# Kernel optimization log

Hardware: AMD Instinct MI355X
Metric: run time of the kernel (lower is better)

## Reference

```python
import jax, jax.numpy as jnp
import numpy as np


def _make_grid(h, w):
    """Replicates gen_grid_coordinates_optimized(h, w, stride=1) vectorized in numpy.
    Returns (h*3, w*3, 2) float32 grid in grid_sample convention (x=col, y=row, in [-1,1])."""
    pi = np.pi
    dphi = pi / h
    dtheta = 2 * pi / w
    tp, tt, icp = np.tan(dphi), np.tan(dtheta), 1.0 / np.cos(dphi)
    xys = np.array([[(-tt, icp * tp), (0, tp), (tt, icp * tp)],
                    [(-tt, 0), (1, 1), (tt, 0)],
                    [(-tt, -icp * tp), (0, -tp), (tt, -icp * tp)]], dtype=np.float64)
    xk, yk = xys[..., 0], xys[..., 1]          # (3,3) kernel offsets on tangent plane
    rho = np.sqrt(xk ** 2 + yk ** 2)
    v = np.arctan(rho)
    cv, sv = np.cos(v), np.sin(v)
    rr = np.arange(h, dtype=np.float64)
    cc = np.arange(w, dtype=np.float64)
    phi = -((rr + 0.5) / h * pi - pi / 2)      # (h,)
    theta = (cc + 0.5) / w * 2 * pi - pi       # (w,)
    cph = np.cos(phi)[:, None, None]
    sph = np.sin(phi)[:, None, None]
    # (h,3,3) ; clip guards fp roundoff at poles (mathematically |arg|<=1)
    new_phi = np.arcsin(np.clip(cv * sph + yk * sv * cph / rho, -1.0, 1.0))
    dtheta_off = np.arctan(xk * sv / (rho * cph * cv - yk * sph * sv))  # (h,3,3)
    new_theta = theta[None, :, None, None] + dtheta_off[:, None]        # (h,w,3,3)
    new_r = np.broadcast_to(((-new_phi + pi / 2) * h / pi - 0.5)[:, None], (h, w, 3, 3)).copy()
    new_c = (new_theta + pi) * w / (2 * pi) - 0.5
    new_c = (new_c + w) % w
    # kernel center samples the pixel itself
    new_r[:, :, 1, 1] = rr[:, None]
    new_c[:, :, 1, 1] = cc[None, :]
    gy = new_r * 2 / h - 1
    gx = new_c * 2 / w - 1
    grid = np.stack([gx, gy], axis=-1)                      # (h,w,ki,kj,2)
    grid = grid.transpose(0, 2, 1, 3, 4).reshape(h * 3, w * 3, 2)
    return grid.astype(np.float32)


def _grid_sample_bilinear(x, grid):
    """F.grid_sample(mode='bilinear', align_corners=True, padding_mode='zeros').
    x: (N,C,H,W), grid: (Hg,Wg,2) shared across batch. Returns (N,C,Hg,Wg)."""
    N, C, H, W = x.shape
    ix = (grid[..., 0] + 1) * 0.5 * (W - 1)
    iy = (grid[..., 1] + 1) * 0.5 * (H - 1)
    x0 = jnp.floor(ix)
    y0 = jnp.floor(iy)
    x1, y1 = x0 + 1, y0 + 1
    xflat = x.reshape(N, C, H * W)

    def corner(yc, xc, wgt):
        valid = (xc >= 0) & (xc <= W - 1) & (yc >= 0) & (yc <= H - 1)
        xi = jnp.clip(xc, 0, W - 1).astype(jnp.int32)
        yi = jnp.clip(yc, 0, H - 1).astype(jnp.int32)
        idx = (yi * W + xi).reshape(-1)
        v = xflat[:, :, idx].reshape(N, C, *xc.shape)
        return v * (wgt * valid)[None, None]

    out = (corner(y0, x0, (x1 - ix) * (y1 - iy))
           + corner(y0, x1, (ix - x0) * (y1 - iy))
           + corner(y1, x0, (x1 - ix) * (iy - y0))
           + corner(y1, x1, (ix - x0) * (iy - y0)))
    return out


def setup_inputs() -> dict:
    key = jax.random.key(0)
    k1, k2 = jax.random.split(key)
    B, Cin, Cout, H, W = 4, 16, 32, 256, 512
    x = jax.random.normal(k1, (B, Cin, H, W), dtype=jnp.float32)
    fan_out = Cout * 9  # kaiming_normal fan_out, relu gain
    weight = jax.random.normal(k2, (Cout, Cin, 3, 3), dtype=jnp.float32) * np.sqrt(2.0 / fan_out)
    bias = jnp.zeros((Cout,), dtype=jnp.float32)
    grid = jnp.asarray(_make_grid(H, W))  # (H*3, W*3, 2) constant spherical warp
    return {"x": x, "weight": weight, "bias": bias, "grid": grid}


def reference(x, weight, bias, grid):
    s = _grid_sample_bilinear(x, grid)  # (N,C,3H,3W)
    out = jax.lax.conv_general_dilated(
        s, weight, window_strides=(3, 3), padding='VALID',
        dimension_numbers=('NCHW', 'OIHW', 'NCHW'))
    return out + bias[None, :, None, None]
```

## Files before the change

### kernel.cpp

```cpp
#include <hip/hip_runtime.h>

#define HH 256
#define WW 512
#define NCIN 16
#define NCOUT 32
#define NB 4
#define WKP 168

typedef _Float16 half8 __attribute__((ext_vector_type(8)));
typedef float f32x16 __attribute__((ext_vector_type(16)));

#define XT_OFF   0u
#define XTAB_OFF 16777216u
#define WTAB_OFF (16777216u + 9437184u)
#define YTAB_OFF (16777216u + 9437184u + 16384u)
#define WS_NEED  (YTAB_OFF + 36864u)

__global__ __launch_bounds__(256) void precompute_all(const float* __restrict__ x,
                                                      const float* __restrict__ w,
                                                      const float* __restrict__ grid,
                                                      _Float16* __restrict__ xh,
                                                      float2* __restrict__ xtab,
                                                      _Float16* __restrict__ wtab,
                                                      float4* __restrict__ ytab) {
    const float2* g2 = reinterpret_cast<const float2*>(grid);
    if (blockIdx.x < 2048) {
        const int lb = (blockIdx.x & 7) * 256 + (blockIdx.x >> 3);
        const int t = lb * 256 + threadIdx.x;
        const int c = t & (WW - 1);
        const int r = (t >> 9) & (HH - 1);
        const int b = t >> 17;
        const float* xp = x + ((size_t)(b * NCIN) * HH + r) * WW + c;
        half8 h0, h1;
#pragma unroll
        for (int ci = 0; ci < 8; ++ci)  h0[ci] = (_Float16)xp[(size_t)ci * (HH * WW)];
#pragma unroll
        for (int ci = 0; ci < 8; ++ci)  h1[ci] = (_Float16)xp[(size_t)(8 + ci) * (HH * WW)];
        half8* op = reinterpret_cast<half8*>(xh) + (size_t)t * 2;
        op[0] = h0;
        op[1] = h1;
        return;
    }
    if (blockIdx.x < 2048 + 4608) {
        const int t = (blockIdx.x - 2048) * 256 + threadIdx.x;
        const int c = t & (WW - 1);
        const int u = t >> 9;
        const int r = u / 9, tap = u - r * 9;
        const int kr = tap / 3, kc = tap - kr * 3;
        const float gx = g2[(size_t)(r * 3 + kr) * (WW * 3) + (c * 3 + kc)].x;
        const float ix = ((gx + 1.0f) * 0.5f) * (float)(WW - 1);
        const float x0f = floorf(ix);
        xtab[t] = make_float2(ix - x0f, __int_as_float((int)x0f));
        return;
    }
    const int t = (blockIdx.x - 6656) * 256 + threadIdx.x;
    if (t < NCOUT * WKP) {
        const int co = t / WKP, kk = t - co * WKP;
        float v = 0.0f;
        if (kk < 144) v = w[co * 144 + (kk & 15) * 9 + (kk >> 4)];
        wtab[t] = (_Float16)v;
    } else if (t < NCOUT * WKP + HH * 9) {
        const int u = t - NCOUT * WKP;
        const int r = u / 9, tap = u - r * 9;
        const int kr = tap / 3, kc = tap - kr * 3;
        const float gy = g2[(size_t)(r * 3 + kr) * (WW * 3) + kc].y;
        const float iy = ((gy + 1.0f) * 0.5f) * (float)(HH - 1);
        const float y0f = floorf(iy);
        const float fy = iy - y0f;
        const int y0 = (int)y0f, y1 = y0 + 1;
        float wy0 = 1.0f - fy, wy1 = fy;
        if (y0 < 0 || y0 > HH - 1) wy0 = 0.0f;
        if (y1 < 0 || y1 > HH - 1) wy1 = 0.0f;
        const int cy0 = min(max(y0, 0), HH - 1), cy1 = min(max(y1, 0), HH - 1);
        ytab[u] = make_float4(wy0, wy1, __int_as_float(cy0), __int_as_float(cy1));
    }
}

__global__ __launch_bounds__(256, 4) void sphere_mfma_kernel(const _Float16* __restrict__ xh,
                                                             const float2* __restrict__ xtab,
                                                             const _Float16* __restrict__ wtab,
                                                             const float4* __restrict__ ytab,
                                                             const float* __restrict__ bias,
                                                             float* __restrict__ out) {
    const int tid = threadIdx.x, lane = tid & 63, wv = tid >> 6;
    const int c32 = lane & 31, h = lane >> 5;
    const int px = wv * 32 + c32;

    const int lb = ((blockIdx.x & 7) << 9) + (blockIdx.x >> 3);
    const int pixbase = lb << 7;
    const int b    = pixbase >> 17;
    const int rimg = (pixbase >> 9) & (HH - 1);
    const int c0   = pixbase & (WW - 1);

    float wy0s[9], wy1s[9];
    int Rb0[9], Rb1[9];
#pragma unroll
    for (int t = 0; t < 9; ++t) {
        const float4 y = ytab[rimg * 9 + t];
        wy0s[t] = y.x;
        wy1s[t] = y.y;
        Rb0[t] = (b * HH + __float_as_int(y.z)) << 10;
        Rb1[t] = (b * HH + __float_as_int(y.w)) << 10;
    }

    const float2* xrow = xtab + (size_t)rimg * 9 * WW + (c0 + px);
    float2 f2s[9];
#pragma unroll
    for (int t = 0; t < 9; ++t) f2s[t] = xrow[t * WW];

    half8 wA[9];
#pragma unroll
    for (int t = 0; t < 9; ++t)
        wA[t] = *reinterpret_cast<const half8*>(wtab + c32 * WKP + t * 16 + h * 8);

    const half8* x8 = reinterpret_cast<const half8*>(xh);
    f32x16 acc = {};
#pragma unroll
    for (int t = 0; t < 9; ++t) {
        const int x0 = __float_as_int(f2s[t].y);
        const int pb0 = Rb0[t] + (x0 << 1) + h;
        const int pb1 = Rb1[t] + (x0 << 1) + h;
        const half8 A00 = x8[pb0];
        const half8 A01 = x8[pb0 + 2];
        const half8 A10 = x8[pb1];
        const half8 A11 = x8[pb1 + 2];

        const float fx = f2s[t].x;
        const float wx0 = 1.0f - fx;
        const float w00 = wx0 * wy0s[t], w01 = fx * wy0s[t];
        const float w10 = wx0 * wy1s[t], w11 = fx * wy1s[t];
        const _Float16 W00 = (_Float16)w00, W01 = (_Float16)w01;
        const _Float16 W10 = (_Float16)w10, W11 = (_Float16)w11;
        const half8 B00 = {W00, W00, W00, W00, W00, W00, W00, W00};
        const half8 B01 = {W01, W01, W01, W01, W01, W01, W01, W01};
        const half8 B10 = {W10, W10, W10, W10, W10, W10, W10, W10};
        const half8 B11 = {W11, W11, W11, W11, W11, W11, W11, W11};
        half8 pk = A00 * B00;
        pk += A01 * B01;
        pk += A10 * B10;
        pk += A11 * B11;

        acc = __builtin_amdgcn_mfma_f32_32x32x16_f16(wA[t], pk, acc, 0, 0, 0);
    }

    const int pix = c0 + wv * 32 + c32;
    float* ob = out + (((size_t)(b * NCOUT) * HH + rimg) * WW) + pix;
#pragma unroll
    for (int reg = 0; reg < 16; ++reg) {
        const int co = (reg & 3) + 8 * (reg >> 2) + 4 * h;
        ob[(size_t)co * (HH * WW)] = acc[reg] + bias[co];
    }
}

__global__ __launch_bounds__(256) void sphere_conv_fallback(const float* __restrict__ x,
                                                            const float* __restrict__ weight,
                                                            const float* __restrict__ bias,
                                                            const float* __restrict__ grid,
                                                            float* __restrict__ out) {
    __shared__ float wlds[NCIN * 9 * NCOUT];
    const int tid = threadIdx.x;
    for (int e = tid; e < NCIN * 9 * NCOUT; e += 256) {
        const int co  = e & (NCOUT - 1);
        const int cik = e >> 5;
        wlds[e] = weight[co * (NCIN * 9) + cik];
    }
    __syncthreads();

    const int pindex = blockIdx.x * 256 + tid;
    const int c = pindex & (WW - 1);
    const int r = (pindex >> 9) & (HH - 1);
    const int b = pindex >> 17;

    float acc[NCOUT];
#pragma unroll
    for (int o = 0; o < NCOUT; ++o) acc[o] = 0.0f;

    const float2* g2 = reinterpret_cast<const float2*>(grid);

#pragma unroll 1
    for (int k = 0; k < 9; ++k) {
        const int kr = k / 3, kc = k - kr * 3;
        const float2 g = g2[(r * 3 + kr) * (WW * 3) + (c * 3 + kc)];
        const float ix = ((g.x + 1.0f) * 0.5f) * (float)(WW - 1);
        const float iy = ((g.y + 1.0f) * 0.5f) * (float)(HH - 1);
        const float x0f = floorf(ix), y0f = floorf(iy);
        const float fx = ix - x0f, fy = iy - y0f;
        const int x0 = (int)x0f, y0 = (int)y0f;
        const int x1 = x0 + 1, y1 = y0 + 1;
        float wx0 = 1.0f - fx, wx1 = fx, wy0 = 1.0f - fy, wy1 = fy;
        if (x0 < 0 || x0 > WW - 1) wx0 = 0.0f;
        if (x1 < 0 || x1 > WW - 1) wx1 = 0.0f;
        if (y0 < 0 || y0 > HH - 1) wy0 = 0.0f;
        if (y1 < 0 || y1 > HH - 1) wy1 = 0.0f;
        const int cx0 = min(max(x0, 0), WW - 1), cx1 = min(max(x1, 0), WW - 1);
        const int cy0 = min(max(y0, 0), HH - 1), cy1 = min(max(y1, 0), HH - 1);
        const float w00 = wx0 * wy0, w01 = wx1 * wy0, w10 = wx0 * wy1, w11 = wx1 * wy1;

#pragma unroll 1
        for (int ci = 0; ci < NCIN; ++ci) {
            const float* xb = x + (size_t)((b * NCIN + ci) * HH) * WW;
            const float a00 = xb[cy0 * WW + cx0];
            const float a01 = xb[cy0 * WW + cx1];
            const float a10 = xb[cy1 * WW + cx0];
            const float a11 = xb[cy1 * WW + cx1];
            const float s = w00 * a00 + w01 * a01 + w10 * a10 + w11 * a11;
            const float4* wl = reinterpret_cast<const float4*>(&wlds[(ci * 9 + k) * NCOUT]);
#pragma unroll
            for (int o = 0; o < 8; ++o) {
                const float4 wv = wl[o];
                acc[o * 4 + 0] += wv.x * s;
                acc[o * 4 + 1] += wv.y * s;
                acc[o * 4 + 2] += wv.z * s;
                acc[o * 4 + 3] += wv.w * s;
            }
        }
    }

    const int obase = ((b * NCOUT) * HH + r) * WW + c;
#pragma unroll
    for (int o = 0; o < NCOUT; ++o) {
        out[obase + o * (HH * WW)] = acc[o] + bias[o];
    }
}

extern "C" void kernel_launch(void* const* d_in, const int* in_sizes, int n_in,
                              void* d_out, int out_size, void* d_ws, size_t ws_size,
                              hipStream_t stream) {
    const float* x    = (const float*)d_in[0];
    const float* w    = (const float*)d_in[1];
    const float* bias = (const float*)d_in[2];
    const float* grid = (const float*)d_in[3];
    float* out = (float*)d_out;

    if (ws_size >= WS_NEED) {
        char* ws = (char*)d_ws;
        _Float16* xh   = (_Float16*)(ws + XT_OFF);
        float2*   xtab = (float2*)(ws + XTAB_OFF);
        _Float16* wtab = (_Float16*)(ws + WTAB_OFF);
        float4*   ytab = (float4*)(ws + YTAB_OFF);

        precompute_all<<<6686, 256, 0, stream>>>(x, w, grid, xh, xtab, wtab, ytab);
        sphere_mfma_kernel<<<4096, 256, 0, stream>>>(xh, xtab, wtab, ytab, bias, out);
    } else {
        sphere_conv_fallback<<<2048, 256, 0, stream>>>(x, w, bias, grid, out);
    }
}
```

Before: 55.40 us.

## Double-buffer gather loads, coalesce grid reads, pre-swizzle MFMA weight fragments

The main kernel's tap loop is now software-pipelined with two register buffers, so the four corner gathers for tap t+2 are issued while tap t is blended and fed to the MFMA. The precompute pass now reads the grid coalesced and scatters into the xtab layout, instead of the strided gather it did before. Weights are also pre-packed into the per-lane MFMA fragment order so each lane does one contiguous half8 load. The pipelining raises register pressure under the 4-blocks-per-CU launch bound, and the xtab writes become scattered.

```diff
diff --git a/kernel.cpp b/kernel.cpp
--- a/kernel.cpp
+++ b/kernel.cpp
@@ -5,14 +5,13 @@
 #define NCIN 16
 #define NCOUT 32
 #define NB 4
-#define WKP 168
 
 typedef _Float16 half8 __attribute__((ext_vector_type(8)));
 typedef float f32x16 __attribute__((ext_vector_type(16)));
 
 #define XT_OFF   0u
 #define XTAB_OFF 16777216u
-#define WTAB_OFF (16777216u + 9437184u)
+#define WFRAG_OFF (16777216u + 9437184u)
 #define YTAB_OFF (16777216u + 9437184u + 16384u)
 #define WS_NEED  (YTAB_OFF + 36864u)
 
@@ -21,7 +20,7 @@
                                                       const float* __restrict__ grid,
                                                       _Float16* __restrict__ xh,
                                                       float2* __restrict__ xtab,
-                                                      _Float16* __restrict__ wtab,
+                                                      _Float16* __restrict__ wfrag,
                                                       float4* __restrict__ ytab) {
     const float2* g2 = reinterpret_cast<const float2*>(grid);
     if (blockIdx.x < 2048) {
@@ -41,29 +40,29 @@
         op[1] = h1;
         return;
     }
-    if (blockIdx.x < 2048 + 4608) {
-        const int t = (blockIdx.x - 2048) * 256 + threadIdx.x;
-        const int c = t & (WW - 1);
-        const int u = t >> 9;
+    if (blockIdx.x < 6656) {
+        const int T = (blockIdx.x - 2048) * 256 + threadIdx.x;
+        const int gr = T / 1536, j = T - gr * 1536;
+        const int r = gr / 3, kr = gr - r * 3;
+        const int c = j / 3, kc = j - c * 3;
+        const float gx = g2[(size_t)gr * 1536 + j].x;
+        const float ix = ((gx + 1.0f) * 0.5f) * (float)(WW - 1);
+        const float x0f = floorf(ix);
+        xtab[(size_t)(r * 9 + kr * 3 + kc) * WW + c] = make_float2(ix - x0f, __int_as_float((int)x0f));
+        return;
+    }
+    if (blockIdx.x < 6674) {
+        const int e = (blockIdx.x - 6656) * 256 + threadIdx.x;
+        const int j = e & 7, lane = (e >> 3) & 63, t = e >> 9;
+        const int c32 = lane & 31, h = lane >> 5;
+        wfrag[e] = (_Float16)w[c32 * 144 + (h * 8 + j) * 9 + t];
+        return;
+    }
+    const int u = (blockIdx.x - 6674) * 256 + threadIdx.x;
+    if (u < HH * 9) {
         const int r = u / 9, tap = u - r * 9;
         const int kr = tap / 3, kc = tap - kr * 3;
-        const float gx = g2[(size_t)(r * 3 + kr) * (WW * 3) + (c * 3 + kc)].x;
-        const float ix = ((gx + 1.0f) * 0.5f) * (float)(WW - 1);
-        const float x0f = floorf(ix);
-        xtab[t] = make_float2(ix - x0f, __int_as_float((int)x0f));
-        return;
-    }
-    const int t = (blockIdx.x - 6656) * 256 + threadIdx.x;
-    if (t < NCOUT * WKP) {
-        const int co = t / WKP, kk = t - co * WKP;
-        float v = 0.0f;
-        if (kk < 144) v = w[co * 144 + (kk & 15) * 9 + (kk >> 4)];
-        wtab[t] = (_Float16)v;
-    } else if (t < NCOUT * WKP + HH * 9) {
-        const int u = t - NCOUT * WKP;
-        const int r = u / 9, tap = u - r * 9;
-        const int kr = tap / 3, kc = tap - kr * 3;
-        const float gy = g2[(size_t)(r * 3 + kr) * (WW * 3) + kc].y;
+        const float gy = g2[(size_t)(r * 3 + kr) * 1536 + kc].y;
         const float iy = ((gy + 1.0f) * 0.5f) * (float)(HH - 1);
         const float y0f = floorf(iy);
         const float fy = iy - y0f;
@@ -78,7 +77,7 @@
 
 __global__ __launch_bounds__(256, 4) void sphere_mfma_kernel(const _Float16* __restrict__ xh,
                                                              const float2* __restrict__ xtab,
-                                                             const _Float16* __restrict__ wtab,
+                                                             const _Float16* __restrict__ wfrag,
                                                              const float4* __restrict__ ytab,
                                                              const float* __restrict__ bias,
                                                              float* __restrict__ out) {
@@ -108,40 +107,59 @@
 #pragma unroll
     for (int t = 0; t < 9; ++t) f2s[t] = xrow[t * WW];
 
+    const half8* wf8 = reinterpret_cast<const half8*>(wfrag);
     half8 wA[9];
 #pragma unroll
-    for (int t = 0; t < 9; ++t)
-        wA[t] = *reinterpret_cast<const half8*>(wtab + c32 * WKP + t * 16 + h * 8);
+    for (int t = 0; t < 9; ++t) wA[t] = wf8[t * 64 + lane];
 
     const half8* x8 = reinterpret_cast<const half8*>(xh);
     f32x16 acc = {};
-#pragma unroll
-    for (int t = 0; t < 9; ++t) {
-        const int x0 = __float_as_int(f2s[t].y);
-        const int pb0 = Rb0[t] + (x0 << 1) + h;
-        const int pb1 = Rb1[t] + (x0 << 1) + h;
-        const half8 A00 = x8[pb0];
-        const half8 A01 = x8[pb0 + 2];
-        const half8 A10 = x8[pb1];
-        const half8 A11 = x8[pb1 + 2];
-
-        const float fx = f2s[t].x;
-        const float wx0 = 1.0f - fx;
-        const float w00 = wx0 * wy0s[t], w01 = fx * wy0s[t];
-        const float w10 = wx0 * wy1s[t], w11 = fx * wy1s[t];
-        const _Float16 W00 = (_Float16)w00, W01 = (_Float16)w01;
-        const _Float16 W10 = (_Float16)w10, W11 = (_Float16)w11;
-        const half8 B00 = {W00, W00, W00, W00, W00, W00, W00, W00};
-        const half8 B01 = {W01, W01, W01, W01, W01, W01, W01, W01};
-        const half8 B10 = {W10, W10, W10, W10, W10, W10, W10, W10};
-        const half8 B11 = {W11, W11, W11, W11, W11, W11, W11, W11};
-        half8 pk = A00 * B00;
-        pk += A01 * B01;
-        pk += A10 * B10;
-        pk += A11 * B11;
-
-        acc = __builtin_amdgcn_mfma_f32_32x32x16_f16(wA[t], pk, acc, 0, 0, 0);
-    }
+
+    half8 A00a, A01a, A10a, A11a, A00b, A01b, A10b, A11b;
+
+#define GLOAD(tt, S)                                                     \
+    {                                                                    \
+        const int x0_ = __float_as_int(f2s[tt].y);                       \
+        const int p0_ = Rb0[tt] + (x0_ << 1) + h;                        \
+        const int p1_ = Rb1[tt] + (x0_ << 1) + h;                        \
+        A00##S = x8[p0_];                                                \
+        A01##S = x8[p0_ + 2];                                            \
+        A10##S = x8[p1_];                                                \
+        A11##S = x8[p1_ + 2];                                            \
+    }
+
+#define CONSUME(tt, S)                                                   \
+    {                                                                    \
+        const float fx_ = f2s[tt].x;                                     \
+        const float wx0_ = 1.0f - fx_;                                   \
+        const float w00_ = wx0_ * wy0s[tt], w01_ = fx_ * wy0s[tt];       \
+        const float w10_ = wx0_ * wy1s[tt], w11_ = fx_ * wy1s[tt];       \
+        const _Float16 W00_ = (_Float16)w00_, W01_ = (_Float16)w01_;     \
+        const _Float16 W10_ = (_Float16)w10_, W11_ = (_Float16)w11_;     \
+        const half8 B00_ = {W00_, W00_, W00_, W00_, W00_, W00_, W00_, W00_}; \
+        const half8 B01_ = {W01_, W01_, W01_, W01_, W01_, W01_, W01_, W01_}; \
+        const half8 B10_ = {W10_, W10_, W10_, W10_, W10_, W10_, W10_, W10_}; \
+        const half8 B11_ = {W11_, W11_, W11_, W11_, W11_, W11_, W11_, W11_}; \
+        half8 pk_ = A00##S * B00_;                                       \
+        pk_ += A01##S * B01_;                                            \
+        pk_ += A10##S * B10_;                                            \
+        pk_ += A11##S * B11_;                                            \
+        acc = __builtin_amdgcn_mfma_f32_32x32x16_f16(wA[tt], pk_, acc, 0, 0, 0); \
+    }
+
+    GLOAD(0, a)
+    GLOAD(1, b)
+    CONSUME(0, a) GLOAD(2, a)
+    CONSUME(1, b) GLOAD(3, b)
+    CONSUME(2, a) GLOAD(4, a)
+    CONSUME(3, b) GLOAD(5, b)
+    CONSUME(4, a) GLOAD(6, a)
+    CONSUME(5, b) GLOAD(7, b)
+    CONSUME(6, a) GLOAD(8, a)
+    CONSUME(7, b)
+    CONSUME(8, a)
+#undef GLOAD
+#undef CONSUME
 
     const int pix = c0 + wv * 32 + c32;
     float* ob = out + (((size_t)(b * NCOUT) * HH + rimg) * WW) + pix;
@@ -234,13 +252,13 @@
 
     if (ws_size >= WS_NEED) {
         char* ws = (char*)d_ws;
-        _Float16* xh   = (_Float16*)(ws + XT_OFF);
-        float2*   xtab = (float2*)(ws + XTAB_OFF);
-        _Float16* wtab = (_Float16*)(ws + WTAB_OFF);
-        float4*   ytab = (float4*)(ws + YTAB_OFF);
-
-        precompute_all<<<6686, 256, 0, stream>>>(x, w, grid, xh, xtab, wtab, ytab);
-        sphere_mfma_kernel<<<4096, 256, 0, stream>>>(xh, xtab, wtab, ytab, bias, out);
+        _Float16* xh    = (_Float16*)(ws + XT_OFF);
+        float2*   xtab  = (float2*)(ws + XTAB_OFF);
+        _Float16* wfrag = (_Float16*)(ws + WFRAG_OFF);
+        float4*   ytab  = (float4*)(ws + YTAB_OFF);
+
+        precompute_all<<<6683, 256, 0, stream>>>(x, w, grid, xh, xtab, wfrag, ytab);
+        sphere_mfma_kernel<<<4096, 256, 0, stream>>>(xh, xtab, wfrag, ytab, bias, out);
     } else {
         sphere_conv_fallback<<<2048, 256, 0, stream>>>(x, w, bias, grid, out);
     }
```

Result: faster. 49.78 us (-10.1%).
